# Kernel tuning notes

Measured on AMD Instinct MI355X. Metric: run time of the kernel, lower is better.

## Reference

```python
import jax, jax.numpy as jnp
import numpy as np

N_NODES = 50000
N_EDGES = 800000
X_DIM = 32
S_DIM = 16
H_DIM = 96   # = 2 * (X_DIM + S_DIM), edge-MLP input
O_DIM = 64


def setup_inputs() -> dict:
    key = jax.random.key(0)
    ks = jax.random.split(key, 6)
    x = jax.random.normal(ks[0], (N_NODES, X_DIM), dtype=jnp.float32)
    scalars = jax.random.normal(ks[1], (1, S_DIM), dtype=jnp.float32)
    W1 = jax.random.normal(ks[2], (H_DIM, H_DIM), dtype=jnp.float32) * (1.0 / np.sqrt(H_DIM))
    b1 = jnp.zeros((H_DIM,), dtype=jnp.float32)
    W2 = jax.random.normal(ks[3], (H_DIM, O_DIM), dtype=jnp.float32) * (1.0 / np.sqrt(H_DIM))
    b2 = jnp.zeros((O_DIM,), dtype=jnp.float32)
    edge_index = jax.random.randint(ks[4], (2, N_EDGES), 0, N_NODES, dtype=jnp.int64)
    return {"x": x, "scalars": scalars, "W1": W1, "b1": b1, "W2": W2,
            "b2": b2, "edge_index": edge_index}


def reference(x, scalars, W1, b1, W2, b2, edge_index):
    n = x.shape[0]
    # single-graph branch of EFN: expand scalars to every node, concat
    s = jnp.broadcast_to(scalars.reshape(1, -1), (n, scalars.shape[-1]))
    h = jnp.concatenate([x, s], axis=1)                      # [N, 48]
    src, dst = edge_index[0], edge_index[1]
    # PTConv: edge-wise MLP on cat([x_i, x_j - x_i]), sum-aggregate to i (dst)
    h_i = h[dst]                                             # [E, 48] gather
    h_j = h[src]                                             # [E, 48] gather
    m_in = jnp.concatenate([h_i, h_j - h_i], axis=1)         # [E, 96]
    m = jax.nn.relu(m_in @ W1 + b1) @ W2 + b2                # [E, 64]
    out = jax.ops.segment_sum(m, dst, num_segments=n)        # [N, 64] scatter-add
    return out
```

## Files before the change

kernel.cpp:

```cpp
#include <hip/hip_runtime.h>


typedef _Float16 half8 __attribute__((ext_vector_type(8)));
typedef _Float16 half2t __attribute__((ext_vector_type(2)));
typedef float f32x4 __attribute__((ext_vector_type(4)));
typedef float f32x2 __attribute__((ext_vector_type(2)));

#define LDK 72
#define LDW2 104
#define LDH 104
#define BCAP 1024
#define NBMAX 1563

static __device__ __forceinline__ unsigned char f32_to_fp8(float v) {
    int p = __builtin_amdgcn_cvt_pk_fp8_f32(v, v, 0, false);
    return (unsigned char)(p & 0xff);
}

__global__ __launch_bounds__(256) void prep_kernel(
    const float* __restrict__ x, const float* __restrict__ scalars,
    const float* __restrict__ W1, const float* __restrict__ b1,
    _Float16* __restrict__ Pbuf, unsigned char* __restrict__ Qf8,
    const int* __restrict__ src, const int* __restrict__ dst,
    int* __restrict__ bcur, unsigned int* __restrict__ pairs,
    int tiles, int n_e4, int epb4, int nb, int nplace)
{
    __shared__ union {
        struct { int h[NBMAX]; int cur[NBMAX]; } pl;
        _Float16 sW[192 * LDK];
    } sm;
    const int tid = threadIdx.x;

    if ((int)blockIdx.x < nplace) {
        int* h = sm.pl.h;
        int* cur = sm.pl.cur;
        for (int b = tid; b < nb; b += 256) h[b] = 0;
        __syncthreads();

        const int base4 = blockIdx.x * epb4;
        for (int i = tid; i < epb4; i += 256) {
            int i4 = base4 + i;
            if (i4 < n_e4) {
                int4 d = ((const int4*)dst)[i4];
                atomicAdd(&h[d.x >> 5], 1);
                atomicAdd(&h[d.y >> 5], 1);
                atomicAdd(&h[d.z >> 5], 1);
                atomicAdd(&h[d.w >> 5], 1);
            }
        }
        __syncthreads();
        for (int b = tid; b < nb; b += 256) {
            int c = h[b];
            cur[b] = b * BCAP + (c ? atomicAdd(&bcur[b], c) : 0);
        }
        __syncthreads();
        for (int i = tid; i < epb4; i += 256) {
            int i4 = base4 + i;
            if (i4 < n_e4) {
                int4 s = ((const int4*)src)[i4];
                int4 d = ((const int4*)dst)[i4];
                int p;
                p = atomicAdd(&cur[d.x >> 5], 1);
                if (p < (d.x >> 5) * BCAP + BCAP) pairs[p] = (unsigned)s.x | ((unsigned)(d.x & 31) << 16);
                p = atomicAdd(&cur[d.y >> 5], 1);
                if (p < (d.y >> 5) * BCAP + BCAP) pairs[p] = (unsigned)s.y | ((unsigned)(d.y & 31) << 16);
                p = atomicAdd(&cur[d.z >> 5], 1);
                if (p < (d.z >> 5) * BCAP + BCAP) pairs[p] = (unsigned)s.z | ((unsigned)(d.z & 31) << 16);
                p = atomicAdd(&cur[d.w >> 5], 1);
                if (p < (d.w >> 5) * BCAP + BCAP) pairs[p] = (unsigned)s.w | ((unsigned)(d.w & 31) << 16);
            }
        }
    } else {
        _Float16* sW = sm.sW;
        for (int idx = tid; idx < 192 * 64; idx += 256) {
            int n = idx >> 6, k = idx & 63;
            float v = 0.f;
            if (k < 48)
                v = (n < 96) ? (W1[k * 96 + n] - W1[(k + 48) * 96 + n])
                             : W1[(k + 48) * 96 + (n - 96)];
            sW[n * LDK + k] = (_Float16)v;
        }
        __syncthreads();

        const int wave = tid >> 6, lane = tid & 63;
        const int quad = lane >> 4, r = lane & 15;
        const int pb = blockIdx.x - nplace;
        const int stride = (gridDim.x - nplace) * 4;

        for (int tile = pb * 4 + wave; tile < tiles; tile += stride) {
            const int node = tile * 16 + r;

            half8 a0, a1;
            {
                const float* xp = x + (size_t)node * 32 + quad * 8;
                #pragma unroll
                for (int j = 0; j < 8; ++j) a0[j] = (_Float16)xp[j];
                #pragma unroll
                for (int j = 0; j < 8; ++j) {
                    int k2 = 32 + quad * 8 + j;
                    a1[j] = (k2 < 48) ? (_Float16)scalars[k2 - 32] : (_Float16)0.f;
                }
            }

            #pragma unroll
            for (int nt = 0; nt < 12; ++nt) {
                f32x4 c = {0.f, 0.f, 0.f, 0.f};
                half8 b0 = *(const half8*)&sW[(nt * 16 + r) * LDK + quad * 8];
                half8 b1v = *(const half8*)&sW[(nt * 16 + r) * LDK + 32 + quad * 8];
                c = __builtin_amdgcn_mfma_f32_16x16x32_f16(a0, b0, c, 0, 0, 0);
                c = __builtin_amdgcn_mfma_f32_16x16x32_f16(a1, b1v, c, 0, 0, 0);
                if (nt < 6) {
                    int col = nt * 16 + r;
                    float bb = b1[col];
                    #pragma unroll
                    for (int i = 0; i < 4; ++i)
                        Pbuf[(size_t)(tile * 16 + quad * 4 + i) * 96 + col] = (_Float16)(c[i] + bb);
                } else {
                    int col = (nt - 6) * 16 + r;
                    #pragma unroll
                    for (int i = 0; i < 4; ++i)
                        Qf8[(size_t)(tile * 16 + quad * 4 + i) * 96 + col] = f32_to_fp8(c[i]);
                }
            }
        }
    }
}

__global__ __launch_bounds__(256) void sgo_kernel(
    const _Float16* __restrict__ Pbuf, const unsigned char* __restrict__ Qf8,
    const int* __restrict__ bcur, const unsigned int* __restrict__ pairs,
    const float* __restrict__ W2, const float* __restrict__ b2,
    float* __restrict__ out, int n_nodes)
{
    __shared__ unsigned int s_pairs[BCAP];
    __shared__ unsigned short s_sorted[BCAP];
    __shared__ _Float16 sW2T[64 * LDW2];
    __shared__ _Float16 sH[32 * LDH];
    __shared__ int s_cnt[32];
    __shared__ int s_off[33];
    __shared__ int s_cur[32];

    const int b = blockIdx.x;
    const int tid = threadIdx.x;
    const int lo_g = b * BCAP;
    int cnt = bcur[b];
    if (cnt > BCAP) cnt = BCAP;

    for (int idx = tid; idx < 96 * 64; idx += 256) {
        int k = idx / 64, n = idx - k * 64;
        sW2T[n * LDW2 + k] = (_Float16)W2[idx];
    }
    if (tid < 32) s_cnt[tid] = 0;
    __syncthreads();

    for (int i = tid; i < cnt; i += 256) {
        unsigned int u = pairs[lo_g + i];
        s_pairs[i] = u;
        atomicAdd(&s_cnt[(u >> 16) & 31], 1);
    }
    __syncthreads();
    if (tid == 0) {
        int a = 0;
        #pragma unroll
        for (int l = 0; l < 32; ++l) { s_off[l] = a; a += s_cnt[l]; }
        s_off[32] = a;
    }
    __syncthreads();
    if (tid < 32) s_cur[tid] = s_off[tid];
    __syncthreads();
    for (int i = tid; i < cnt; i += 256) {
        unsigned int u = s_pairs[i];
        int p = atomicAdd(&s_cur[(u >> 16) & 31], 1);
        s_sorted[p] = (unsigned short)(u & 0xffffu);
    }
    __syncthreads();

    const int wave = tid >> 6, lane = tid & 63;
    const int g = lane >> 3, j = lane & 7;

    for (int ni = wave * 8; ni < wave * 8 + 8; ++ni) {
        const int node = b * 32 + ni;
        const int lo = s_off[ni], hi = s_off[ni + 1];

        float pf[12];
        {
            const unsigned int* Pp = (const unsigned int*)(Pbuf + (size_t)node * 96);
            #pragma unroll
            for (int t = 0; t < 6; ++t) {
                half2t h = __builtin_bit_cast(half2t, Pp[j * 6 + t]);
                pf[2 * t] = (float)h[0];
                pf[2 * t + 1] = (float)h[1];
            }
        }

        float ac[12];
        #pragma unroll
        for (int k = 0; k < 12; ++k) ac[k] = 0.f;

        for (int i = lo + g; i < hi; i += 8) {
            int s = s_sorted[i];
            const unsigned int* Qp = (const unsigned int*)(Qf8 + (size_t)s * 96);
            unsigned int q0 = Qp[j * 3 + 0];
            unsigned int q1 = Qp[j * 3 + 1];
            unsigned int q2 = Qp[j * 3 + 2];
            f32x2 v;
            v = __builtin_amdgcn_cvt_pk_f32_fp8((int)q0, false);
            { float t0 = pf[0] + v[0], t1 = pf[1] + v[1];
              ac[0] += t0 > 0.f ? t0 : 0.f; ac[1] += t1 > 0.f ? t1 : 0.f; }
            v = __builtin_amdgcn_cvt_pk_f32_fp8((int)q0, true);
            { float t0 = pf[2] + v[0], t1 = pf[3] + v[1];
              ac[2] += t0 > 0.f ? t0 : 0.f; ac[3] += t1 > 0.f ? t1 : 0.f; }
            v = __builtin_amdgcn_cvt_pk_f32_fp8((int)q1, false);
            { float t0 = pf[4] + v[0], t1 = pf[5] + v[1];
              ac[4] += t0 > 0.f ? t0 : 0.f; ac[5] += t1 > 0.f ? t1 : 0.f; }
            v = __builtin_amdgcn_cvt_pk_f32_fp8((int)q1, true);
            { float t0 = pf[6] + v[0], t1 = pf[7] + v[1];
              ac[6] += t0 > 0.f ? t0 : 0.f; ac[7] += t1 > 0.f ? t1 : 0.f; }
            v = __builtin_amdgcn_cvt_pk_f32_fp8((int)q2, false);
            { float t0 = pf[8] + v[0], t1 = pf[9] + v[1];
              ac[8] += t0 > 0.f ? t0 : 0.f; ac[9] += t1 > 0.f ? t1 : 0.f; }
            v = __builtin_amdgcn_cvt_pk_f32_fp8((int)q2, true);
            { float t0 = pf[10] + v[0], t1 = pf[11] + v[1];
              ac[10] += t0 > 0.f ? t0 : 0.f; ac[11] += t1 > 0.f ? t1 : 0.f; }
        }

        #pragma unroll
        for (int m = 8; m < 64; m <<= 1)
            #pragma unroll
            for (int k = 0; k < 12; ++k)
                ac[k] += __shfl_xor(ac[k], m);

        if (g == 0) {
            unsigned int* Hp = (unsigned int*)(sH + (size_t)ni * LDH);
            #pragma unroll
            for (int t = 0; t < 6; ++t) {
                half2t hv;
                hv[0] = (_Float16)ac[2 * t];
                hv[1] = (_Float16)ac[2 * t + 1];
                Hp[j * 6 + t] = __builtin_bit_cast(unsigned int, hv);
            }
        }
    }
    __syncthreads();

    const int quad = lane >> 4, r = lane & 15;
    const int t = wave >> 1;
    const int nt0 = (wave & 1) * 2;

    half8 a[3];
    #pragma unroll
    for (int kk = 0; kk < 3; ++kk)
        a[kk] = *(const half8*)&sH[(t * 16 + r) * LDH + kk * 32 + quad * 8];

    #pragma unroll
    for (int w = 0; w < 2; ++w) {
        const int nt = nt0 + w;
        f32x4 c = {0.f, 0.f, 0.f, 0.f};
        #pragma unroll
        for (int kk = 0; kk < 3; ++kk) {
            half8 bfrag = *(const half8*)&sW2T[(nt * 16 + r) * LDW2 + kk * 32 + quad * 8];
            c = __builtin_amdgcn_mfma_f32_16x16x32_f16(a[kk], bfrag, c, 0, 0, 0);
        }
        const int col = nt * 16 + r;
        const float bb = b2[col];
        #pragma unroll
        for (int i = 0; i < 4; ++i) {
            int local = t * 16 + quad * 4 + i;
            int node = b * 32 + local;
            if (node < n_nodes) {
                int dg = s_off[local + 1] - s_off[local];
                out[(size_t)node * 64 + col] = c[i] + dg * bb;
            }
        }
    }
}

extern "C" void kernel_launch(void* const* d_in, const int* in_sizes, int n_in,
                              void* d_out, int out_size, void* d_ws, size_t ws_size,
                              hipStream_t stream) {
    const float* x       = (const float*)d_in[0];
    const float* scalars = (const float*)d_in[1];
    const float* W1      = (const float*)d_in[2];
    const float* b1      = (const float*)d_in[3];
    const float* W2      = (const float*)d_in[4];
    const float* b2      = (const float*)d_in[5];
    const int*   ei      = (const int*)d_in[6];
    float* out = (float*)d_out;

    const int n_edges = in_sizes[6] / 2;
    const int n_nodes = in_sizes[0] / 32;
    const int* src = ei;
    const int* dst = ei + n_edges;
    const int nb = (n_nodes + 31) / 32;
    const int tiles = n_nodes / 16;

    char* w = (char*)d_ws;
    _Float16* Pbuf = (_Float16*)w;          w += (size_t)n_nodes * 96 * 2;
    unsigned char* Qf8 = (unsigned char*)w; w += (size_t)n_nodes * 96;
    unsigned int* pairs = (unsigned int*)w; w += (size_t)nb * BCAP * 4;
    int* bcur = (int*)w;                    w += (size_t)nb * 4;

    hipMemsetAsync(bcur, 0, (size_t)nb * 4, stream);

    const int nplace = 128;
    const int n_e4 = n_edges / 4;
    const int epb4 = (n_e4 + nplace - 1) / nplace;
    prep_kernel<<<dim3(256), dim3(256), 0, stream>>>(
        x, scalars, W1, b1, Pbuf, Qf8, src, dst, bcur, pairs,
        tiles, n_e4, epb4, nb, nplace);

    sgo_kernel<<<dim3(nb), dim3(256), 0, stream>>>(
        Pbuf, Qf8, bcur, pairs, W2, b2, out, n_nodes);
}
```

Measured before the change: 143.0 us.

## Assign one node per 8-lane group in aggregation, drop shuffle reduction and pair staging

The aggregation loop now gives each 8-lane group its own node, so the wave handles 8 nodes at once instead of looping over them with groups striding edges. This removes the cross-group shuffle reduction and the serial per-node loop. The inner loop is unrolled by two edges to expose more independent loads. The LDS staging of pairs is dropped in favour of reading them from global memory twice, and the placement block count in prep is raised. Load imbalance across groups with different degrees may now add divergence.

```diff
diff --git a/kernel.cpp b/kernel.cpp
--- a/kernel.cpp
+++ b/kernel.cpp
@@ -126,13 +126,37 @@
     }
 }
 
+static __device__ __forceinline__ void acc_edge(
+    float* __restrict__ ac, const float* __restrict__ pf,
+    unsigned int q0, unsigned int q1, unsigned int q2)
+{
+    f32x2 v;
+    v = __builtin_amdgcn_cvt_pk_f32_fp8((int)q0, false);
+    { float t0 = pf[0] + v[0], t1 = pf[1] + v[1];
+      ac[0] += t0 > 0.f ? t0 : 0.f; ac[1] += t1 > 0.f ? t1 : 0.f; }
+    v = __builtin_amdgcn_cvt_pk_f32_fp8((int)q0, true);
+    { float t0 = pf[2] + v[0], t1 = pf[3] + v[1];
+      ac[2] += t0 > 0.f ? t0 : 0.f; ac[3] += t1 > 0.f ? t1 : 0.f; }
+    v = __builtin_amdgcn_cvt_pk_f32_fp8((int)q1, false);
+    { float t0 = pf[4] + v[0], t1 = pf[5] + v[1];
+      ac[4] += t0 > 0.f ? t0 : 0.f; ac[5] += t1 > 0.f ? t1 : 0.f; }
+    v = __builtin_amdgcn_cvt_pk_f32_fp8((int)q1, true);
+    { float t0 = pf[6] + v[0], t1 = pf[7] + v[1];
+      ac[6] += t0 > 0.f ? t0 : 0.f; ac[7] += t1 > 0.f ? t1 : 0.f; }
+    v = __builtin_amdgcn_cvt_pk_f32_fp8((int)q2, false);
+    { float t0 = pf[8] + v[0], t1 = pf[9] + v[1];
+      ac[8] += t0 > 0.f ? t0 : 0.f; ac[9] += t1 > 0.f ? t1 : 0.f; }
+    v = __builtin_amdgcn_cvt_pk_f32_fp8((int)q2, true);
+    { float t0 = pf[10] + v[0], t1 = pf[11] + v[1];
+      ac[10] += t0 > 0.f ? t0 : 0.f; ac[11] += t1 > 0.f ? t1 : 0.f; }
+}
+
 __global__ __launch_bounds__(256) void sgo_kernel(
     const _Float16* __restrict__ Pbuf, const unsigned char* __restrict__ Qf8,
     const int* __restrict__ bcur, const unsigned int* __restrict__ pairs,
     const float* __restrict__ W2, const float* __restrict__ b2,
     float* __restrict__ out, int n_nodes)
 {
-    __shared__ unsigned int s_pairs[BCAP];
     __shared__ unsigned short s_sorted[BCAP];
     __shared__ _Float16 sW2T[64 * LDW2];
     __shared__ _Float16 sH[32 * LDH];
@@ -153,23 +177,20 @@
     if (tid < 32) s_cnt[tid] = 0;
     __syncthreads();
 
+    for (int i = tid; i < cnt; i += 256)
+        atomicAdd(&s_cnt[(pairs[lo_g + i] >> 16) & 31], 1);
+    __syncthreads();
+    if (tid == 0) {
+        int a = 0;
+        #pragma unroll
+        for (int l = 0; l < 32; ++l) { s_off[l] = a; a += s_cnt[l]; }
+        s_off[32] = a;
+    }
+    __syncthreads();
+    if (tid < 32) s_cur[tid] = s_off[tid];
+    __syncthreads();
     for (int i = tid; i < cnt; i += 256) {
         unsigned int u = pairs[lo_g + i];
-        s_pairs[i] = u;
-        atomicAdd(&s_cnt[(u >> 16) & 31], 1);
-    }
-    __syncthreads();
-    if (tid == 0) {
-        int a = 0;
-        #pragma unroll
-        for (int l = 0; l < 32; ++l) { s_off[l] = a; a += s_cnt[l]; }
-        s_off[32] = a;
-    }
-    __syncthreads();
-    if (tid < 32) s_cur[tid] = s_off[tid];
-    __syncthreads();
-    for (int i = tid; i < cnt; i += 256) {
-        unsigned int u = s_pairs[i];
         int p = atomicAdd(&s_cur[(u >> 16) & 31], 1);
         s_sorted[p] = (unsigned short)(u & 0xffffu);
     }
@@ -177,9 +198,10 @@
 
     const int wave = tid >> 6, lane = tid & 63;
     const int g = lane >> 3, j = lane & 7;
-
-    for (int ni = wave * 8; ni < wave * 8 + 8; ++ni) {
-        const int node = b * 32 + ni;
+    const int ni = wave * 8 + g;
+    const int node = b * 32 + ni;
+
+    if (node < n_nodes) {
         const int lo = s_off[ni], hi = s_off[ni + 1];
 
         float pf[12];
@@ -197,48 +219,30 @@
         #pragma unroll
         for (int k = 0; k < 12; ++k) ac[k] = 0.f;
 
-        for (int i = lo + g; i < hi; i += 8) {
-            int s = s_sorted[i];
-            const unsigned int* Qp = (const unsigned int*)(Qf8 + (size_t)s * 96);
-            unsigned int q0 = Qp[j * 3 + 0];
-            unsigned int q1 = Qp[j * 3 + 1];
-            unsigned int q2 = Qp[j * 3 + 2];
-            f32x2 v;
-            v = __builtin_amdgcn_cvt_pk_f32_fp8((int)q0, false);
-            { float t0 = pf[0] + v[0], t1 = pf[1] + v[1];
-              ac[0] += t0 > 0.f ? t0 : 0.f; ac[1] += t1 > 0.f ? t1 : 0.f; }
-            v = __builtin_amdgcn_cvt_pk_f32_fp8((int)q0, true);
-            { float t0 = pf[2] + v[0], t1 = pf[3] + v[1];
-              ac[2] += t0 > 0.f ? t0 : 0.f; ac[3] += t1 > 0.f ? t1 : 0.f; }
-            v = __builtin_amdgcn_cvt_pk_f32_fp8((int)q1, false);
-            { float t0 = pf[4] + v[0], t1 = pf[5] + v[1];
-              ac[4] += t0 > 0.f ? t0 : 0.f; ac[5] += t1 > 0.f ? t1 : 0.f; }
-            v = __builtin_amdgcn_cvt_pk_f32_fp8((int)q1, true);
-            { float t0 = pf[6] + v[0], t1 = pf[7] + v[1];
-              ac[6] += t0 > 0.f ? t0 : 0.f; ac[7] += t1 > 0.f ? t1 : 0.f; }
-            v = __builtin_amdgcn_cvt_pk_f32_fp8((int)q2, false);
-            { float t0 = pf[8] + v[0], t1 = pf[9] + v[1];
-              ac[8] += t0 > 0.f ? t0 : 0.f; ac[9] += t1 > 0.f ? t1 : 0.f; }
-            v = __builtin_amdgcn_cvt_pk_f32_fp8((int)q2, true);
-            { float t0 = pf[10] + v[0], t1 = pf[11] + v[1];
-              ac[10] += t0 > 0.f ? t0 : 0.f; ac[11] += t1 > 0.f ? t1 : 0.f; }
-        }
-
-        #pragma unroll
-        for (int m = 8; m < 64; m <<= 1)
-            #pragma unroll
-            for (int k = 0; k < 12; ++k)
-                ac[k] += __shfl_xor(ac[k], m);
-
-        if (g == 0) {
-            unsigned int* Hp = (unsigned int*)(sH + (size_t)ni * LDH);
-            #pragma unroll
-            for (int t = 0; t < 6; ++t) {
-                half2t hv;
-                hv[0] = (_Float16)ac[2 * t];
-                hv[1] = (_Float16)ac[2 * t + 1];
-                Hp[j * 6 + t] = __builtin_bit_cast(unsigned int, hv);
-            }
+        int i = lo;
+        for (; i + 1 < hi; i += 2) {
+            int s0 = s_sorted[i];
+            int s1 = s_sorted[i + 1];
+            const unsigned int* Q0 = (const unsigned int*)(Qf8 + (size_t)s0 * 96);
+            const unsigned int* Q1 = (const unsigned int*)(Qf8 + (size_t)s1 * 96);
+            unsigned int a0 = Q0[j * 3 + 0], a1 = Q0[j * 3 + 1], a2 = Q0[j * 3 + 2];
+            unsigned int c0 = Q1[j * 3 + 0], c1 = Q1[j * 3 + 1], c2 = Q1[j * 3 + 2];
+            acc_edge(ac, pf, a0, a1, a2);
+            acc_edge(ac, pf, c0, c1, c2);
+        }
+        if (i < hi) {
+            int s0 = s_sorted[i];
+            const unsigned int* Q0 = (const unsigned int*)(Qf8 + (size_t)s0 * 96);
+            acc_edge(ac, pf, Q0[j * 3 + 0], Q0[j * 3 + 1], Q0[j * 3 + 2]);
+        }
+
+        unsigned int* Hp = (unsigned int*)sH + ni * (LDH / 2);
+        #pragma unroll
+        for (int t = 0; t < 6; ++t) {
+            half2t hv;
+            hv[0] = (_Float16)ac[2 * t];
+            hv[1] = (_Float16)ac[2 * t + 1];
+            Hp[j * 6 + t] = __builtin_bit_cast(unsigned int, hv);
         }
     }
     __syncthreads();
@@ -266,10 +270,10 @@
         #pragma unroll
         for (int i = 0; i < 4; ++i) {
             int local = t * 16 + quad * 4 + i;
-            int node = b * 32 + local;
-            if (node < n_nodes) {
+            int nd = b * 32 + local;
+            if (nd < n_nodes) {
                 int dg = s_off[local + 1] - s_off[local];
-                out[(size_t)node * 64 + col] = c[i] + dg * bb;
+                out[(size_t)nd * 64 + col] = c[i] + dg * bb;
             }
         }
     }
@@ -302,7 +306,7 @@
 
     hipMemsetAsync(bcur, 0, (size_t)nb * 4, stream);
 
-    const int nplace = 128;
+    const int nplace = 160;
     const int n_e4 = n_edges / 4;
     const int epb4 = (n_e4 + nplace - 1) / nplace;
     prep_kernel<<<dim3(256), dim3(256), 0, stream>>>(
```

Result: faster. 126.3 us, median of 2 (-11.6%).
